# Optimization experiments

Hardware: AMD Instinct MI355X
Metric: run time of the kernel (lower is better)

The kernel has to match this reference:

```python
import jax, jax.numpy as jnp
import numpy as np

MIN_LOGITS_VALUE = -2.3819763e+38
MAX_WAVELENGTH = 10000


def _apply_rope(inputs, positions):
    # inputs: [b, t, n, h]; positions: [b, t]. RoPE on first half of h.
    x_rope, x = jnp.split(inputs, 2, axis=-1)
    pos = positions[:, :, None, None].astype(jnp.float32)  # [b, t, 1, 1]
    freq_exponents = 2.0 * jnp.arange(x_rope.shape[-1] // 2) / x_rope.shape[-1]
    inv_freq = 1.0 / (MAX_WAVELENGTH ** freq_exponents)
    sinusoid = pos * inv_freq  # [b, t, 1, h/2]
    sin = jnp.sin(sinusoid).astype(inputs.dtype)
    cos = jnp.cos(sinusoid).astype(inputs.dtype)
    first, second = jnp.split(x_rope, 2, axis=-1)
    return jnp.concatenate(
        [first * cos - second * sin, second * cos + first * sin, x], axis=-1)


def _forward_pass_mask(segment_pos, window_size):
    # segment_pos: [b, t]; 0 marks a segment start.
    segment_ids = jnp.cumsum(segment_pos == 0, axis=-1)  # [b, t]
    t = segment_pos.shape[-1]
    positions = jnp.arange(t)
    same_segment = segment_ids[:, :, None] == segment_ids[:, None, :]
    causal = positions[:, None] >= positions[None, :]
    window = positions[:, None] <= positions[None, :] + window_size
    return same_segment & (causal & window)[None]  # [b, t, t]


def setup_inputs() -> dict:
    key = jax.random.key(0)
    ks = jax.random.split(key, 6)
    B, T, W, N = 2, 2048, 2048, 16
    H = W // N
    x = jax.random.normal(ks[0], (B, T, W), jnp.float32)
    sc = 1.0 / np.sqrt(W).astype(np.float32)
    w_q = jax.random.normal(ks[1], (W, W), jnp.float32) * sc
    w_k = jax.random.normal(ks[2], (W, H), jnp.float32) * sc
    w_v = jax.random.normal(ks[3], (W, H), jnp.float32) * sc
    w_out = jax.random.normal(ks[4], (W, W), jnp.float32) * sc
    b_out = jnp.zeros((W,), jnp.float32)
    segment_pos = jnp.tile(jnp.arange(T, dtype=jnp.int32)[None], (B, 1))
    return {"x": x, "w_q": w_q, "w_k": w_k, "w_v": w_v, "w_out": w_out,
            "b_out": b_out, "segment_pos": segment_pos,
            "num_heads": N, "window_size": 1024}


def reference(x, w_q, w_k, w_v, w_out, b_out, segment_pos, num_heads, window_size):
    b, t, width = x.shape
    head_dim = width // num_heads
    # Projections: MQA -> keys/values are single-head [b, t, head_dim].
    q = (x @ w_q).reshape(b, t, num_heads, head_dim)
    k = (x @ w_k)[:, :, None, :]  # [b, t, 1, h]
    v = x @ w_v                   # [b, t, h]
    q = _apply_rope(q, segment_pos)
    k = _apply_rope(k, segment_pos)[:, :, 0]  # [b, t, h]
    logits = jnp.einsum('btnh,bsh->bnts', q, k) * (head_dim ** -0.5)
    mask = _forward_pass_mask(segment_pos, window_size)  # [b, t, t]
    masked = jnp.where(mask[:, None], logits, MIN_LOGITS_VALUE).astype(jnp.float32)
    probs = jax.nn.softmax(masked, axis=-1).astype(x.dtype)
    encoded = jnp.einsum('bnts,bsh->btnh', probs, v).reshape(b, t, width)
    return encoded @ w_out + b_out
```

## Files before the change

### kernel.cpp

```cpp
#include <hip/hip_runtime.h>
#include <hip/hip_bf16.h>
#include <stdint.h>

typedef __attribute__((ext_vector_type(8))) short short8;
typedef __attribute__((ext_vector_type(4))) float f32x4;

__device__ __forceinline__ float bf2f(short u) {
  return __uint_as_float(((unsigned)(unsigned short)u) << 16);
}
__device__ __forceinline__ short f2bf(float f) {
  unsigned x = __float_as_uint(f);
  unsigned r = (x + 0x7fffu + ((x >> 16) & 1u)) >> 16;
  return (short)r;
}

__device__ __forceinline__ void gload_lds16(const short* g, short* l) {
  __builtin_amdgcn_global_load_lds(
      (const __attribute__((address_space(1))) void*)g,
      (__attribute__((address_space(3))) void*)l, 16, 0, 0);
}

__global__ void cast_x_bf16(const float* __restrict__ in, short* __restrict__ out, int n8) {
  int i = blockIdx.x * blockDim.x + threadIdx.x;
  if (i >= n8) return;
  const float4* p = (const float4*)in + (size_t)i * 2;
  float4 a = p[0], b = p[1];
  short8 o;
  o[0] = f2bf(a.x); o[1] = f2bf(a.y); o[2] = f2bf(a.z); o[3] = f2bf(a.w);
  o[4] = f2bf(b.x); o[5] = f2bf(b.y); o[6] = f2bf(b.z); o[7] = f2bf(b.w);
  *((short8*)out + i) = o;
}

__global__ void transpose_cast(const float* __restrict__ in, int R, int C,
                               short* __restrict__ out, int row_off, int ldo) {
  __shared__ float tile[32][33];
  int c0 = blockIdx.x * 32, r0 = blockIdx.y * 32;
  int tx = threadIdx.x, ty = threadIdx.y;
#pragma unroll
  for (int i = 0; i < 4; ++i)
    tile[ty + i * 8][tx] = in[(size_t)(r0 + ty + i * 8) * C + (c0 + tx)];
  __syncthreads();
#pragma unroll
  for (int i = 0; i < 4; ++i)
    out[(size_t)(row_off + c0 + ty + i * 8) * ldo + (r0 + tx)] =
        f2bf(tile[tx][ty + i * 8]);
}

template <int OUT_F32>
__global__ __launch_bounds__(256)
void gemm_bt(const short* __restrict__ A, const short* __restrict__ Bt,
             int M, int N, int K, int ldc,
             short* __restrict__ outb, float* __restrict__ outf,
             const float* __restrict__ bias) {
  __shared__ short As[128 * 64];
  __shared__ short Bs[128 * 64];
  const int tid = threadIdx.x, lane = tid & 63;
  const int wr = tid >> 7, wc = (tid >> 6) & 1;
  const int l15 = lane & 15, l4 = lane >> 4;
  const int m0 = blockIdx.y * 128, n0 = blockIdx.x * 128;
  f32x4 acc[4][4] = {};
  for (int k0 = 0; k0 < K; k0 += 64) {
#pragma unroll
    for (int iss = 0; iss < 4; ++iss) {
      int c = iss * 256 + tid;
      int row = c >> 3, q = c & 7;
      gload_lds16(A + (size_t)(m0 + row) * K + k0 + q * 8,
                  As + iss * 2048 + (tid & 192) * 8);
      gload_lds16(Bt + (size_t)(n0 + row) * K + k0 + q * 8,
                  Bs + iss * 2048 + (tid & 192) * 8);
    }
    __syncthreads();
#pragma unroll
    for (int kk = 0; kk < 2; ++kk) {
      short8 a[4], b[4];
#pragma unroll
      for (int mi = 0; mi < 4; ++mi)
        a[mi] = *(const short8*)(As + (wr * 64 + mi * 16 + l15) * 64 + kk * 32 + l4 * 8);
#pragma unroll
      for (int ni = 0; ni < 4; ++ni)
        b[ni] = *(const short8*)(Bs + (wc * 64 + ni * 16 + l15) * 64 + kk * 32 + l4 * 8);
#pragma unroll
      for (int mi = 0; mi < 4; ++mi)
#pragma unroll
        for (int ni = 0; ni < 4; ++ni)
          acc[mi][ni] = __builtin_amdgcn_mfma_f32_16x16x32_bf16(a[mi], b[ni], acc[mi][ni], 0, 0, 0);
    }
    __syncthreads();
  }
#pragma unroll
  for (int mi = 0; mi < 4; ++mi)
#pragma unroll
    for (int ni = 0; ni < 4; ++ni)
#pragma unroll
      for (int r = 0; r < 4; ++r) {
        int row = m0 + wr * 64 + mi * 16 + l4 * 4 + r;
        int col = n0 + wc * 64 + ni * 16 + l15;
        if (OUT_F32)
          outf[(size_t)row * ldc + col] = acc[mi][ni][r] + bias[col];
        else
          outb[(size_t)row * ldc + col] = f2bf(acc[mi][ni][r]);
      }
}

__global__ void rope_kernel(short* __restrict__ qkv, const int* __restrict__ segpos,
                            int nheads, int hd, int ld) {
  const int row = blockIdx.x;
  const float pos = (float)segpos[row];
  short* base = qkv + (size_t)row * ld;
  const int quarter = hd >> 2;
  const int npairs_q = nheads * quarter;
  const int total = npairs_q + quarter;
  for (int p = threadIdx.x; p < total; p += blockDim.x) {
    int i, off;
    if (p < npairs_q) { off = (p >> 5) * hd; i = p & 31; }
    else              { off = nheads * hd;  i = p - npairs_q; }
    float ang = pos * exp2f(-(float)i * (13.287712379549449f / (float)quarter));
    float s, c;
    sincosf(ang, &s, &c);
    float a = bf2f(base[off + i]);
    float b = bf2f(base[off + quarter + i]);
    base[off + i]           = f2bf(a * c - b * s);
    base[off + quarter + i] = f2bf(b * c + a * s);
  }
}

__global__ __launch_bounds__(256)
void attn_kernel(const short* __restrict__ qkv, short* __restrict__ enc,
                 const int* __restrict__ wsz_p, int T, int nheads) {
  const int window = wsz_p[0];
  const int qt = blockIdx.x;
  const int bh = blockIdx.y;
  const int b = bh / nheads, n = bh % nheads;
  const int tid = threadIdx.x, lane = tid & 63, w = tid >> 6;
  const int l15 = lane & 15, l4 = lane >> 4;
  const int q0 = qt * 64;
  const size_t rowbase = (size_t)b * T;
  const int LD = nheads * 128 + 256;
  const int kcol = nheads * 128;
  const float CC = 0.08838834764831845f * 1.4426950408889634f;

  __shared__ short Ks[64 * 128];
  __shared__ short Vt[128 * 64];
  __shared__ short Pl[4][16 * 72];

  short8 qf[4];
  {
    const short* qptr = qkv + (rowbase + q0 + w * 16 + l15) * LD + n * 128 + l4 * 8;
#pragma unroll
    for (int kk = 0; kk < 4; ++kk) qf[kk] = *(const short8*)(qptr + kk * 32);
  }
  f32x4 o[8] = {};
  float mrow[4], lrow[4];
#pragma unroll
  for (int r = 0; r < 4; ++r) { mrow[r] = -1e30f; lrow[r] = 0.f; }

  int st_lo = q0 - window; if (st_lo < 0) st_lo = 0; st_lo >>= 6;
  const int st_hi = q0 >> 6;
  for (int st = st_lo; st <= st_hi; ++st) {
    const int s0 = st * 64;
#pragma unroll
    for (int it = 0; it < 4; ++it) {
      int c = it * 256 + tid;
      int r = c >> 4, col8 = (c & 15) * 8;
      short8 kv = *(const short8*)(qkv + (rowbase + s0 + r) * LD + kcol + col8);
      int byt = (r * 256 + col8 * 2) ^ ((r & 7) << 4);
      *(short8*)((char*)Ks + byt) = kv;
    }
#pragma unroll
    for (int it = 0; it < 4; ++it) {
      int c = it * 256 + tid;
      int h = c & 127, s8 = (c >> 7) * 8;
      const short* vp = qkv + (rowbase + s0 + s8) * LD + kcol + 128 + h;
      short8 vv;
#pragma unroll
      for (int j = 0; j < 8; ++j) vv[j] = vp[(size_t)j * LD];
      int byt = (h * 128 + s8 * 2) ^ ((h & 7) << 4);
      *(short8*)((char*)Vt + byt) = vv;
    }
    __syncthreads();
    f32x4 sacc[4];
#pragma unroll
    for (int si = 0; si < 4; ++si) {
      f32x4 acc = {};
      int srow = si * 16 + l15;
#pragma unroll
      for (int kk = 0; kk < 4; ++kk) {
        int byt = (srow * 256 + (kk * 32 + l4 * 8) * 2) ^ ((srow & 7) << 4);
        short8 kf = *(const short8*)((const char*)Ks + byt);
        acc = __builtin_amdgcn_mfma_f32_16x16x32_bf16(qf[kk], kf, acc, 0, 0, 0);
      }
      sacc[si] = acc;
    }
    const int trow0 = q0 + w * 16 + l4 * 4;
    float mt[4];
#pragma unroll
    for (int r = 0; r < 4; ++r) mt[r] = -1e30f;
#pragma unroll
    for (int si = 0; si < 4; ++si) {
      int s = s0 + si * 16 + l15;
#pragma unroll
      for (int r = 0; r < 4; ++r) {
        int t = trow0 + r;
        float v = (s <= t && t <= s + window) ? sacc[si][r] : -1e30f;
        sacc[si][r] = v;
        mt[r] = fmaxf(mt[r], v);
      }
    }
#pragma unroll
    for (int r = 0; r < 4; ++r)
#pragma unroll
      for (int off = 1; off < 16; off <<= 1)
        mt[r] = fmaxf(mt[r], __shfl_xor(mt[r], off));
    float fac[4], psum[4];
#pragma unroll
    for (int r = 0; r < 4; ++r) {
      float mnew = fmaxf(mrow[r], mt[r]);
      fac[r] = exp2f((mrow[r] - mnew) * CC);
      mrow[r] = mnew;
      psum[r] = 0.f;
    }
#pragma unroll
    for (int si = 0; si < 4; ++si)
#pragma unroll
      for (int r = 0; r < 4; ++r) {
        float p = exp2f((sacc[si][r] - mrow[r]) * CC);
        psum[r] += p;
        Pl[w][(l4 * 4 + r) * 72 + si * 16 + l15] = f2bf(p);
      }
#pragma unroll
    for (int r = 0; r < 4; ++r) {
#pragma unroll
      for (int off = 1; off < 16; off <<= 1)
        psum[r] += __shfl_xor(psum[r], off);
      lrow[r] = lrow[r] * fac[r] + psum[r];
    }
#pragma unroll
    for (int nt = 0; nt < 8; ++nt)
#pragma unroll
      for (int r = 0; r < 4; ++r) o[nt][r] *= fac[r];
#pragma unroll
    for (int kk = 0; kk < 2; ++kk) {
      short8 pf = *(const short8*)(&Pl[w][l15 * 72 + kk * 32 + l4 * 8]);
#pragma unroll
      for (int nt = 0; nt < 8; ++nt) {
        int h = nt * 16 + l15;
        int byt = (h * 128 + (kk * 32 + l4 * 8) * 2) ^ ((h & 7) << 4);
        short8 vf = *(const short8*)((const char*)Vt + byt);
        o[nt] = __builtin_amdgcn_mfma_f32_16x16x32_bf16(pf, vf, o[nt], 0, 0, 0);
      }
    }
    __syncthreads();
  }
#pragma unroll
  for (int nt = 0; nt < 8; ++nt)
#pragma unroll
    for (int r = 0; r < 4; ++r) {
      size_t row = rowbase + q0 + w * 16 + l4 * 4 + r;
      int col = n * 128 + nt * 16 + l15;
      enc[row * (size_t)(nheads * 128) + col] = f2bf(o[nt][r] / lrow[r]);
    }
}

extern "C" void kernel_launch(void* const* d_in, const int* in_sizes, int n_in,
                              void* d_out, int out_size, void* d_ws, size_t ws_size,
                              hipStream_t stream) {
  const float* x     = (const float*)d_in[0];
  const float* w_q   = (const float*)d_in[1];
  const float* w_k   = (const float*)d_in[2];
  const float* w_v   = (const float*)d_in[3];
  const float* w_out = (const float*)d_in[4];
  const float* b_out = (const float*)d_in[5];
  const int* segpos  = (const int*)d_in[6];
  const int* wsz     = (const int*)d_in[8];
  float* out = (float*)d_out;

  const int BT = in_sizes[6];
  const int W  = in_sizes[5];
  const int H  = in_sizes[2] / W;
  const int NH = W / H;
  const int T  = 2048;
  const int NQKV = W + 2 * H;

  char* ws = (char*)d_ws;
  short* xb    = (short*)ws;
  short* wqkvT = (short*)(ws + (size_t)BT * W * 2);
  short* woutT = (short*)(ws + (size_t)(BT * W + NQKV * W) * 2);
  short* qkv   = (short*)(ws + (size_t)(BT * W + NQKV * W + W * W) * 2);
  short* enc   = xb;

  int n8 = BT * W / 8;
  cast_x_bf16<<<(n8 + 255) / 256, 256, 0, stream>>>(x, xb, n8);

  dim3 tb(32, 8);
  transpose_cast<<<dim3(W / 32, W / 32), tb, 0, stream>>>(w_q, W, W, wqkvT, 0, W);
  transpose_cast<<<dim3(H / 32, W / 32), tb, 0, stream>>>(w_k, W, H, wqkvT, W, W);
  transpose_cast<<<dim3(H / 32, W / 32), tb, 0, stream>>>(w_v, W, H, wqkvT, W + H, W);
  transpose_cast<<<dim3(W / 32, W / 32), tb, 0, stream>>>(w_out, W, W, woutT, 0, W);

  gemm_bt<0><<<dim3(NQKV / 128, BT / 128), 256, 0, stream>>>(
      xb, wqkvT, BT, NQKV, W, NQKV, qkv, nullptr, nullptr);

  rope_kernel<<<BT, 256, 0, stream>>>(qkv, segpos, NH, H, NQKV);

  attn_kernel<<<dim3(T / 64, (BT / T) * NH), 256, 0, stream>>>(qkv, enc, wsz, T, NH);

  gemm_bt<1><<<dim3(W / 128, BT / 128), 256, 0, stream>>>(
      enc, woutT, BT, W, W, W, nullptr, out, b_out);
}
```

Before: 379.7 us.

## Restructure attention: 128-row query tiles, register-prefetched K/V, lazy rescale

The attention kernel moves to 512-thread blocks covering 128 query rows, so each K/V tile loaded into shared memory serves twice as many queries. The next K/V tile is prefetched into registers while the current one is computed, and the V transpose now uses coalesced row loads with a new XOR swizzle. Blocks are linearized with the heaviest query tiles scheduled first. Warps skip tiles outside their mask, the softmax rescale is skipped when the running max grows by no more than a threshold, and MFMA sections get raised wave priority. The costs are higher register pressure, scalar short stores into shared memory for V, and an extra barrier per tile.

```diff
diff --git a/kernel.cpp b/kernel.cpp
--- a/kernel.cpp
+++ b/kernel.cpp
@@ -124,16 +124,18 @@
   }
 }
 
-__global__ __launch_bounds__(256)
+#define SWZV(h) ((((h) ^ ((h) >> 3)) & 7) << 4)
+__global__ __launch_bounds__(512, 4)
 void attn_kernel(const short* __restrict__ qkv, short* __restrict__ enc,
-                 const int* __restrict__ wsz_p, int T, int nheads) {
+                 const int* __restrict__ wsz_p, int T, int nheads, int nqt, int bhc) {
   const int window = wsz_p[0];
-  const int qt = blockIdx.x;
-  const int bh = blockIdx.y;
+  const int i = blockIdx.x;
+  const int qt = nqt - 1 - (i / bhc);
+  const int bh = i % bhc;
   const int b = bh / nheads, n = bh % nheads;
   const int tid = threadIdx.x, lane = tid & 63, w = tid >> 6;
   const int l15 = lane & 15, l4 = lane >> 4;
-  const int q0 = qt * 64;
+  const int q0 = qt * 128;
   const size_t rowbase = (size_t)b * T;
   const int LD = nheads * 128 + 256;
   const int kcol = nheads * 128;
@@ -141,7 +143,7 @@
 
   __shared__ short Ks[64 * 128];
   __shared__ short Vt[128 * 64];
-  __shared__ short Pl[4][16 * 72];
+  __shared__ short Pl[8][16 * 72];
 
   short8 qf[4];
   {
@@ -154,103 +156,142 @@
 #pragma unroll
   for (int r = 0; r < 4; ++r) { mrow[r] = -1e30f; lrow[r] = 0.f; }
 
+  const int tmin = q0 + w * 16, tmax = tmin + 15;
   int st_lo = q0 - window; if (st_lo < 0) st_lo = 0; st_lo >>= 6;
-  const int st_hi = q0 >> 6;
+  const int st_hi = (q0 + 127) >> 6;
+
+  short8 kreg[2], vreg[2];
+  auto load_tile = [&](int s0) {
+#pragma unroll
+    for (int it = 0; it < 2; ++it) {
+      int c = it * 512 + tid;
+      int r = c >> 4, cg = c & 15;
+      const short* rowp = qkv + (rowbase + s0 + r) * (size_t)LD + kcol;
+      kreg[it] = *(const short8*)(rowp + cg * 8);
+      vreg[it] = *(const short8*)(rowp + 128 + cg * 8);
+    }
+  };
+  auto store_tile = [&]() {
+#pragma unroll
+    for (int it = 0; it < 2; ++it) {
+      int c = it * 512 + tid;
+      int r = c >> 4, cg = c & 15;
+      *(short8*)((char*)Ks + ((r * 256 + cg * 16) ^ ((r & 7) << 4))) = kreg[it];
+      int h0 = cg * 8;
+#pragma unroll
+      for (int j = 0; j < 8; ++j) {
+        int h = h0 + j;
+        *(short*)((char*)Vt + ((h * 128 + r * 2) ^ SWZV(h))) = vreg[it][j];
+      }
+    }
+  };
+
+  load_tile(st_lo * 64);
+  store_tile();
+  __syncthreads();
+
   for (int st = st_lo; st <= st_hi; ++st) {
     const int s0 = st * 64;
-#pragma unroll
-    for (int it = 0; it < 4; ++it) {
-      int c = it * 256 + tid;
-      int r = c >> 4, col8 = (c & 15) * 8;
-      short8 kv = *(const short8*)(qkv + (rowbase + s0 + r) * LD + kcol + col8);
-      int byt = (r * 256 + col8 * 2) ^ ((r & 7) << 4);
-      *(short8*)((char*)Ks + byt) = kv;
-    }
-#pragma unroll
-    for (int it = 0; it < 4; ++it) {
-      int c = it * 256 + tid;
-      int h = c & 127, s8 = (c >> 7) * 8;
-      const short* vp = qkv + (rowbase + s0 + s8) * LD + kcol + 128 + h;
-      short8 vv;
-#pragma unroll
-      for (int j = 0; j < 8; ++j) vv[j] = vp[(size_t)j * LD];
-      int byt = (h * 128 + s8 * 2) ^ ((h & 7) << 4);
-      *(short8*)((char*)Vt + byt) = vv;
+    const bool more = (st < st_hi);
+    if (more) load_tile(s0 + 64);
+
+    const bool active = (s0 <= tmax) && (tmin <= s0 + 63 + window);
+    if (active) {
+      f32x4 sacc[4];
+      __builtin_amdgcn_s_setprio(1);
+#pragma unroll
+      for (int si = 0; si < 4; ++si) {
+        f32x4 acc = {};
+        int srow = si * 16 + l15;
+#pragma unroll
+        for (int kk = 0; kk < 4; ++kk) {
+          int byt = (srow * 256 + (kk * 32 + l4 * 8) * 2) ^ ((srow & 7) << 4);
+          short8 kf = *(const short8*)((const char*)Ks + byt);
+          acc = __builtin_amdgcn_mfma_f32_16x16x32_bf16(qf[kk], kf, acc, 0, 0, 0);
+        }
+        sacc[si] = acc;
+      }
+      __builtin_amdgcn_s_setprio(0);
+
+      const int trow0 = q0 + w * 16 + l4 * 4;
+      float mt[4];
+#pragma unroll
+      for (int r = 0; r < 4; ++r) mt[r] = -1e30f;
+#pragma unroll
+      for (int si = 0; si < 4; ++si) {
+        int s = s0 + si * 16 + l15;
+#pragma unroll
+        for (int r = 0; r < 4; ++r) {
+          int t = trow0 + r;
+          float v = (s <= t && t <= s + window) ? sacc[si][r] : -1e30f;
+          sacc[si][r] = v;
+          mt[r] = fmaxf(mt[r], v);
+        }
+      }
+#pragma unroll
+      for (int r = 0; r < 4; ++r)
+#pragma unroll
+        for (int off = 1; off < 16; off <<= 1)
+          mt[r] = fmaxf(mt[r], __shfl_xor(mt[r], off));
+
+      bool dfr = true;
+#pragma unroll
+      for (int r = 0; r < 4; ++r) dfr = dfr && ((mt[r] - mrow[r]) * CC <= 8.0f);
+      const bool defer = __all(dfr);
+      float fac[4];
+      if (!defer) {
+#pragma unroll
+        for (int r = 0; r < 4; ++r) {
+          float mnew = fmaxf(mrow[r], mt[r]);
+          fac[r] = exp2f((mrow[r] - mnew) * CC);
+          mrow[r] = mnew;
+        }
+      }
+      float psum[4];
+#pragma unroll
+      for (int r = 0; r < 4; ++r) psum[r] = 0.f;
+#pragma unroll
+      for (int si = 0; si < 4; ++si)
+#pragma unroll
+        for (int r = 0; r < 4; ++r) {
+          float p = exp2f((sacc[si][r] - mrow[r]) * CC);
+          psum[r] += p;
+          Pl[w][(l4 * 4 + r) * 72 + si * 16 + l15] = f2bf(p);
+        }
+#pragma unroll
+      for (int r = 0; r < 4; ++r) {
+#pragma unroll
+        for (int off = 1; off < 16; off <<= 1)
+          psum[r] += __shfl_xor(psum[r], off);
+        if (!defer) lrow[r] = lrow[r] * fac[r] + psum[r];
+        else        lrow[r] += psum[r];
+      }
+      if (!defer) {
+#pragma unroll
+        for (int nt = 0; nt < 8; ++nt)
+#pragma unroll
+          for (int r = 0; r < 4; ++r) o[nt][r] *= fac[r];
+      }
+
+      __builtin_amdgcn_s_setprio(1);
+#pragma unroll
+      for (int kk = 0; kk < 2; ++kk) {
+        short8 pf = *(const short8*)(&Pl[w][l15 * 72 + kk * 32 + l4 * 8]);
+#pragma unroll
+        for (int nt = 0; nt < 8; ++nt) {
+          int h = nt * 16 + l15;
+          int vb = (h * 128 + kk * 64 + l4 * 16) ^ SWZV(h);
+          short8 vf = *(const short8*)((const char*)Vt + vb);
+          o[nt] = __builtin_amdgcn_mfma_f32_16x16x32_bf16(pf, vf, o[nt], 0, 0, 0);
+        }
+      }
+      __builtin_amdgcn_s_setprio(0);
     }
     __syncthreads();
-    f32x4 sacc[4];
-#pragma unroll
-    for (int si = 0; si < 4; ++si) {
-      f32x4 acc = {};
-      int srow = si * 16 + l15;
-#pragma unroll
-      for (int kk = 0; kk < 4; ++kk) {
-        int byt = (srow * 256 + (kk * 32 + l4 * 8) * 2) ^ ((srow & 7) << 4);
-        short8 kf = *(const short8*)((const char*)Ks + byt);
-        acc = __builtin_amdgcn_mfma_f32_16x16x32_bf16(qf[kk], kf, acc, 0, 0, 0);
-      }
-      sacc[si] = acc;
-    }
-    const int trow0 = q0 + w * 16 + l4 * 4;
-    float mt[4];
-#pragma unroll
-    for (int r = 0; r < 4; ++r) mt[r] = -1e30f;
-#pragma unroll
-    for (int si = 0; si < 4; ++si) {
-      int s = s0 + si * 16 + l15;
-#pragma unroll
-      for (int r = 0; r < 4; ++r) {
-        int t = trow0 + r;
-        float v = (s <= t && t <= s + window) ? sacc[si][r] : -1e30f;
-        sacc[si][r] = v;
-        mt[r] = fmaxf(mt[r], v);
-      }
-    }
-#pragma unroll
-    for (int r = 0; r < 4; ++r)
-#pragma unroll
-      for (int off = 1; off < 16; off <<= 1)
-        mt[r] = fmaxf(mt[r], __shfl_xor(mt[r], off));
-    float fac[4], psum[4];
-#pragma unroll
-    for (int r = 0; r < 4; ++r) {
-      float mnew = fmaxf(mrow[r], mt[r]);
-      fac[r] = exp2f((mrow[r] - mnew) * CC);
-      mrow[r] = mnew;
-      psum[r] = 0.f;
-    }
-#pragma unroll
-    for (int si = 0; si < 4; ++si)
-#pragma unroll
-      for (int r = 0; r < 4; ++r) {
-        float p = exp2f((sacc[si][r] - mrow[r]) * CC);
-        psum[r] += p;
-        Pl[w][(l4 * 4 + r) * 72 + si * 16 + l15] = f2bf(p);
-      }
-#pragma unroll
-    for (int r = 0; r < 4; ++r) {
-#pragma unroll
-      for (int off = 1; off < 16; off <<= 1)
-        psum[r] += __shfl_xor(psum[r], off);
-      lrow[r] = lrow[r] * fac[r] + psum[r];
-    }
-#pragma unroll
-    for (int nt = 0; nt < 8; ++nt)
-#pragma unroll
-      for (int r = 0; r < 4; ++r) o[nt][r] *= fac[r];
-#pragma unroll
-    for (int kk = 0; kk < 2; ++kk) {
-      short8 pf = *(const short8*)(&Pl[w][l15 * 72 + kk * 32 + l4 * 8]);
-#pragma unroll
-      for (int nt = 0; nt < 8; ++nt) {
-        int h = nt * 16 + l15;
-        int byt = (h * 128 + (kk * 32 + l4 * 8) * 2) ^ ((h & 7) << 4);
-        short8 vf = *(const short8*)((const char*)Vt + byt);
-        o[nt] = __builtin_amdgcn_mfma_f32_16x16x32_bf16(pf, vf, o[nt], 0, 0, 0);
-      }
-    }
+    if (more) store_tile();
     __syncthreads();
   }
+
 #pragma unroll
   for (int nt = 0; nt < 8; ++nt)
 #pragma unroll
@@ -302,7 +343,9 @@
 
   rope_kernel<<<BT, 256, 0, stream>>>(qkv, segpos, NH, H, NQKV);
 
-  attn_kernel<<<dim3(T / 64, (BT / T) * NH), 256, 0, stream>>>(qkv, enc, wsz, T, NH);
+  const int nqt = T / 128;
+  const int bhc = (BT / T) * NH;
+  attn_kernel<<<nqt * bhc, 512, 0, stream>>>(qkv, enc, wsz, T, NH, nqt, bhc);
 
   gemm_bt<1><<<dim3(W / 128, BT / 128), 256, 0, stream>>>(
       enc, woutT, BT, W, W, W, nullptr, out, b_out);
```

Result: slower. 520.7 us (+37.1%).
